# Performance work log

Hardware: AMD Instinct MI355X
Metric: run time of the kernel (lower is better)

The kernel has to match this reference:

```python
import jax, jax.numpy as jnp
import numpy as np
import math

IN_C, OUT_C, KH, KW = 128, 128, 3, 3
GROUPS_NUM, NUM_W = 8, 8
STRIDE, PAD, DIL = 1, 1, 1
BETA = 1.0


def setup_inputs() -> dict:
    key = jax.random.key(0)
    ks = jax.random.split(key, 6)
    B, H, W = 8, 56, 56
    n = IN_C * KH * KW
    bound = math.sqrt(6.0 / n)  # reset_parameters bound for weight templates
    inputs = jax.random.normal(ks[0], (B, IN_C, H, W), jnp.float32)
    mask = jax.random.randint(ks[1], (B, H, W), 0, GROUPS_NUM)
    Alpha = jax.random.uniform(ks[2], (B, GROUPS_NUM, H, W), jnp.float32)
    weight_templates = jax.random.uniform(ks[3], (OUT_C * IN_C * KH * KW, NUM_W), jnp.float32, -bound, bound)
    routing_w = jax.random.normal(ks[4], (GROUPS_NUM * NUM_W, IN_C), jnp.float32) * 0.01
    routing_b = jnp.zeros((GROUPS_NUM * NUM_W,), jnp.float32)
    bias = jnp.zeros((OUT_C,), jnp.float32)
    return dict(inputs=inputs, mask=mask, Alpha=Alpha, weight_templates=weight_templates,
                routing_w=routing_w, routing_b=routing_b, bias=bias, use_alpha=1)


def _unfold(x):
    # torch F.unfold-compatible im2col: [B, C*KH*KW, Ho, Wo], channel-major feature order
    return jax.lax.conv_general_dilated_patches(
        x, (KH, KW), (STRIDE, STRIDE), [(PAD, PAD), (PAD, PAD)],
        rhs_dilation=(DIL, DIL), dimension_numbers=('NCHW', 'OIHW', 'NCHW'))


def reference(inputs, mask, Alpha, weight_templates, routing_w, routing_b, bias, use_alpha):
    B, C, H, W = inputs.shape
    K = IN_C * KH * KW
    # SE-style routing: GAP -> fc -> scaled sigmoid (alpha=1.0 in source)
    x_se = inputs.reshape(B, C, -1).mean(-1)                              # [B, C]
    x_se = 2.0 * jax.nn.sigmoid(x_se @ routing_w.T + routing_b) / NUM_W   # [B, G*num_W]
    # blend weight templates: F.linear(x_se.reshape(-1,num_W), weight)
    w = x_se.reshape(B * GROUPS_NUM, NUM_W) @ weight_templates.T          # [B*G, O*K]
    w = w.reshape(B, GROUPS_NUM, OUT_C, K).transpose(0, 2, 3, 1)          # [B, O, K, G]
    patches = _unfold(inputs)                                             # [B, K, Ho, Wo]
    # per-group convolution outputs, then per-pixel group routing
    y = jnp.einsum('bokg,bkhw->boghw', w, patches)                        # [B, O, G, Ho, Wo]
    if use_alpha:
        probs = jax.nn.softmax(BETA * Alpha, axis=1)                      # soft routing [B, G, Ho, Wo]
    else:
        probs = jax.nn.one_hot(mask, GROUPS_NUM, axis=1, dtype=y.dtype)   # hard per-pixel group select
    out = jnp.einsum('boghw,bghw->bohw', y, probs)
    return out + bias.reshape(1, -1, 1, 1)
```

## Files before the change

### kernel.cpp

```cpp
#include <hip/hip_runtime.h>
#include <stdint.h>

#define IN_C   128
#define OUT_C  128
#define KTOT   1152
#define NG     8
#define NW     8
#define NB     8
#define HH     56
#define WWID   56
#define NPIX   3136
#define PPAD   3200
#define MTOT   1024
#define HALO   58
#define HPIX   (HALO*HALO)


typedef __attribute__((ext_vector_type(8))) short short8;
typedef __attribute__((ext_vector_type(8))) unsigned short ushort8;
typedef __attribute__((ext_vector_type(4))) float f32x4;

__device__ __forceinline__ unsigned short f2bf(float f) {
    unsigned u = __float_as_uint(f);
    u += 0x7FFF + ((u >> 16) & 1);
    return (unsigned short)(u >> 16);
}

__device__ __forceinline__ void cp16(const unsigned short* g, unsigned short* l) {
    __builtin_amdgcn_global_load_lds(
        (const __attribute__((address_space(1))) unsigned int*)g,
        (__attribute__((address_space(3))) unsigned int*)l,
        16, 0, 0);
}

__global__ __launch_bounds__(256) void prep_kernel(const float* __restrict__ in,
                                                   const float* __restrict__ T,
                                                   float* __restrict__ xse,
                                                   unsigned short* __restrict__ Apack,
                                                   unsigned short* __restrict__ Xt) {
    __shared__ __align__(16) unsigned char smem[32768];
    const int blk = blockIdx.x;
    const int t = threadIdx.x;

    if (blk < 1024) {
        const float* src = in + (size_t)blk * NPIX;
        float s = 0.f;
        for (int i = t; i < NPIX / 4; i += 256) {
            float4 v = ((const float4*)src)[i];
            s += v.x + v.y + v.z + v.w;
        }
        #pragma unroll
        for (int off = 32; off; off >>= 1) s += __shfl_down(s, off);
        float* ws4 = (float*)smem;
        if ((t & 63) == 0) ws4[t >> 6] = s;
        __syncthreads();
        if (t == 0)
            xse[blk] = (ws4[0] + ws4[1] + ws4[2] + ws4[3]) * (1.0f / (float)NPIX);
        return;
    }
    if (blk < 1152) {
        unsigned short* lh = (unsigned short*)smem;
        const int o = blk - 1024;
        const float* To = T + (size_t)o * 9216;
        #pragma unroll
        for (int it = 0; it < 9; it++) {
            const int f = it * 256 + t;
            const float4 v = ((const float4*)To)[f];
            ushort4 h;
            h.x = f2bf(v.x); h.y = f2bf(v.y); h.z = f2bf(v.z); h.w = f2bf(v.w);
            *(ushort4*)&lh[f * 4] = h;
        }
        __syncthreads();
        const int m16b = o >> 1;
        const int lrb = (o & 1) * 8;
        #pragma unroll
        for (int it = 0; it < 5; it++) {
            const int ch = it * 256 + t;
            if (ch < 1152) {
                const int j = ch & 7, kc = ch >> 3;
                const int s = kc >> 4, c0 = (kc & 15) << 3;
                const int kt = kc >> 2, lq = kc & 3;
                ushort8 v;
                #pragma unroll
                for (int i = 0; i < 8; i++)
                    v[i] = lh[((c0 + i) * 9 + s) * 8 + j];
                const size_t off = ((((size_t)m16b * 36 + kt) * 4 + lq) * 16 + lrb + j) * 8;
                *(ushort8*)&Apack[off] = v;
            }
        }
        return;
    }
    unsigned short* tile = (unsigned short*)smem;
    const int idx = blk - 1152;
    const int yt = idx % 28;
    const int b  = idx / 28;
    const int y0 = yt * 2;

    #pragma unroll
    for (int it = 0; it < 14; it++) {
        const int f = it * 256 + t;
        const int c = f / 28;
        const int rem = f - c * 28;
        const int y = rem / 14;
        const int x4 = rem - y * 14;
        const float4 v = *(const float4*)(in + ((size_t)(b * IN_C + c)) * NPIX
                                          + (y0 + y) * WWID + x4 * 4);
        unsigned short bf0 = f2bf(v.x), bf1 = f2bf(v.y), bf2 = f2bf(v.z), bf3 = f2bf(v.w);
        const int ppb = (y * WWID + x4 * 4) ^ (((c >> 3) & 15) << 2);
        uint2 pk;
        pk.x = (unsigned)bf0 | ((unsigned)bf1 << 16);
        pk.y = (unsigned)bf2 | ((unsigned)bf3 << 16);
        *(uint2*)&tile[c * 128 + ppb] = pk;
    }
    __syncthreads();

    #pragma unroll
    for (int it = 0; it < 7; it++) {
        const int ch = it * 256 + t;
        const int oct = ch & 15;
        const int pp = ch >> 4;
        const int sw = oct << 2;
        ushort8 v;
        #pragma unroll
        for (int i = 0; i < 8; i++)
            v[i] = tile[(oct * 8 + i) * 128 + (pp ^ sw)];
        const int y2 = (pp >= WWID) ? 1 : 0;
        const int xg = pp - y2 * WWID;
        const size_t hp = (size_t)b * HPIX + (y0 + y2 + 1) * HALO + (xg + 1);
        *(ushort8*)&Xt[hp * 128 + oct * 8] = v;
    }

    if (t < 64) {
        const int pi = t >> 4, oct = t & 15;
        const int yy = y0 + 1 + (pi >> 1);
        const int xx = (pi & 1) * 57;
        *(ushort8*)&Xt[((size_t)b * HPIX + yy * HALO + xx) * 128 + oct * 8] =
            (ushort8){0, 0, 0, 0, 0, 0, 0, 0};
    }
    if (yt == 0 || yt == 27) {
        const int yy = (yt == 0) ? 0 : 57;
        #pragma unroll
        for (int it = 0; it < 4; it++) {
            const int ch = it * 256 + t;
            if (ch < 928) {
                const int xx = ch >> 4, oct = ch & 15;
                *(ushort8*)&Xt[((size_t)b * HPIX + yy * HALO + xx) * 128 + oct * 8] =
                    (ushort8){0, 0, 0, 0, 0, 0, 0, 0};
            }
        }
    }
}

__global__ __launch_bounds__(256) void s_kernel(const float* __restrict__ Alpha,
                                                const int* __restrict__ mask,
                                                const float* __restrict__ xse,
                                                const float* __restrict__ rw,
                                                const float* __restrict__ rb,
                                                const int* __restrict__ use_alpha,
                                                float* __restrict__ Sws) {
    const int b = blockIdx.y;
    const int t = threadIdx.x;
    const int p = blockIdx.x * 256 + t;
    __shared__ float xs[IN_C];
    __shared__ float rsh[64];
    if (t < IN_C) xs[t] = xse[b * IN_C + t];
    __syncthreads();
    if (t < 64) {
        float acc = rb[t];
        #pragma unroll 8
        for (int c = 0; c < IN_C; c++) acc += xs[c] * rw[t * IN_C + c];
        rsh[t] = 0.25f / (1.0f + expf(-acc));
    }
    __syncthreads();
    if (p >= PPAD) return;
    float sj[8] = {0, 0, 0, 0, 0, 0, 0, 0};
    if (p < NPIX) {
        float pr[8];
        if (use_alpha[0]) {
            float a[8], m = -1e30f;
            #pragma unroll
            for (int g = 0; g < 8; g++) {
                a[g] = Alpha[((size_t)(b * NG + g)) * NPIX + p];
                m = fmaxf(m, a[g]);
            }
            float sum = 0.f;
            #pragma unroll
            for (int g = 0; g < 8; g++) { pr[g] = expf(a[g] - m); sum += pr[g]; }
            float inv = 1.f / sum;
            #pragma unroll
            for (int g = 0; g < 8; g++) pr[g] *= inv;
        } else {
            int mg = mask[(size_t)b * NPIX + p];
            #pragma unroll
            for (int g = 0; g < 8; g++) pr[g] = (g == mg) ? 1.f : 0.f;
        }
        #pragma unroll
        for (int g = 0; g < 8; g++)
            #pragma unroll
            for (int j = 0; j < 8; j++) sj[j] += pr[g] * rsh[g * 8 + j];
    }
    float* dst = Sws + ((size_t)b * PPAD + p) * 8;
    *(f32x4*)dst = (f32x4){sj[0], sj[1], sj[2], sj[3]};
    *(f32x4*)(dst + 4) = (f32x4){sj[4], sj[5], sj[6], sj[7]};
}

__global__ __launch_bounds__(256) void gemm_kernel(const unsigned short* __restrict__ Apack,
                                                   const unsigned short* __restrict__ Xt,
                                                   const float* __restrict__ Sws,
                                                   const float* __restrict__ bias,
                                                   float* __restrict__ out) {
    __shared__ __align__(16) unsigned short Bsh[4][512 * 8];
    const int tid = threadIdx.x;
    const int wv = tid >> 6, ln = tid & 63;
    const int lq = ln >> 4, lr = ln & 15;
    const int wrow = wv >> 1, wcol = wv & 1;

    const int lid = blockIdx.x;
    const int b   = lid & 7;
    const int sl  = lid >> 3;
    const int mt  = sl & 7;
    const int nt  = sl >> 3;

    f32x4 acc[4][4];
    #pragma unroll
    for (int i = 0; i < 4; i++)
        #pragma unroll
        for (int j = 0; j < 4; j++) acc[i][j] = (f32x4){0.f, 0.f, 0.f, 0.f};

    const int js = tid & 3;
    const int r0 = tid >> 2,  q0 = js ^ (r0 & 3) ^ ((r0 >> 2) & 3);
    const int r1 = r0 + 64,   q1 = js ^ (r1 & 3) ^ ((r1 >> 2) & 3);
    const int p0 = min(nt * 128 + r0, NPIX - 1);
    const int p1 = min(nt * 128 + r1, NPIX - 1);
    const int y0p = p0 / WWID, x0p = p0 - y0p * WWID;
    const int y1p = p1 / WWID, x1p = p1 - y1p * WWID;
    const unsigned short* gb0 = Xt + ((size_t)b * HPIX + y0p * HALO + x0p) * 128 + q0 * 8;
    const unsigned short* gb1 = Xt + ((size_t)b * HPIX + y1p * HALO + x1p) * 128 + q1 * 8;
    unsigned short* lbA[4];
    #pragma unroll
    for (int i = 0; i < 4; i++) lbA[i] = &Bsh[i][(wv * 64) * 8];

    const unsigned short* gaw[4];
    #pragma unroll
    for (int tm = 0; tm < 4; tm++) {
        const int m16 = mt * 8 + wrow * 4 + tm;
        gaw[tm] = Apack + ((size_t)m16 * 36 * 64 + ln) * 8;
    }

    const int jj = lq ^ (lr & 3) ^ ((lr >> 2) & 3);

    cp16(gb0, lbA[0]); cp16(gb1, lbA[0] + 256 * 8);
    cp16(gb0 + 32, lbA[1]); cp16(gb1 + 32, lbA[1] + 256 * 8);
    short8 af[2][4];
    #pragma unroll
    for (int tm = 0; tm < 4; tm++) af[0][tm] = *(const short8*)(gaw[tm]);
    #pragma unroll
    for (int tm = 0; tm < 4; tm++) af[1][tm] = *(const short8*)(gaw[tm] + 512);

    #pragma unroll 1
    for (int pr = 0; pr < 18; pr++) {
        __syncthreads();
        const int st2 = pr * 2 + 2, st3 = pr * 2 + 3;
        if (pr < 17) {
            const int nk2 = st2 * 32, s2 = nk2 >> 7;
            const int kh2 = s2 / 3, kw2 = s2 - 3 * kh2;
            const int off2 = (kh2 * HALO + kw2) * 128 + (nk2 & 127);
            const int nk3 = st3 * 32, s3 = nk3 >> 7;
            const int kh3 = s3 / 3, kw3 = s3 - 3 * kh3;
            const int off3 = (kh3 * HALO + kw3) * 128 + (nk3 & 127);
            unsigned short* d2 = lbA[st2 & 3];
            unsigned short* d3 = lbA[st3 & 3];
            cp16(gb0 + off2, d2); cp16(gb1 + off2, d2 + 256 * 8);
            cp16(gb0 + off3, d3); cp16(gb1 + off3, d3 + 256 * 8);
        }
        const int bufa = (pr & 1) * 2;
        {
            short8 bfr[4];
            #pragma unroll
            for (int tn = 0; tn < 4; tn++) {
                const int row = wcol * 64 + tn * 16 + lr;
                bfr[tn] = *(const short8*)&Bsh[bufa][(row * 4 + jj) * 8];
            }
            #pragma unroll
            for (int tm = 0; tm < 4; tm++)
                #pragma unroll
                for (int tn = 0; tn < 4; tn++)
                    acc[tm][tn] = __builtin_amdgcn_mfma_f32_16x16x32_bf16(
                        af[0][tm], bfr[tn], acc[tm][tn], 0, 0, 0);
        }
        if (pr < 17) {
            #pragma unroll
            for (int tm = 0; tm < 4; tm++)
                af[0][tm] = *(const short8*)(gaw[tm] + (size_t)st2 * 512);
        }
        {
            short8 bfr[4];
            #pragma unroll
            for (int tn = 0; tn < 4; tn++) {
                const int row = wcol * 64 + tn * 16 + lr;
                bfr[tn] = *(const short8*)&Bsh[bufa + 1][(row * 4 + jj) * 8];
            }
            #pragma unroll
            for (int tm = 0; tm < 4; tm++)
                #pragma unroll
                for (int tn = 0; tn < 4; tn++)
                    acc[tm][tn] = __builtin_amdgcn_mfma_f32_16x16x32_bf16(
                        af[1][tm], bfr[tn], acc[tm][tn], 0, 0, 0);
        }
        if (pr < 17) {
            #pragma unroll
            for (int tm = 0; tm < 4; tm++)
                af[1][tm] = *(const short8*)(gaw[tm] + (size_t)st3 * 512);
        }
    }

    const int j0 = (lq & 1) * 4;
    const int oo = lq >> 1;
    #pragma unroll
    for (int tm = 0; tm < 4; tm++) {
        const int o = mt * 16 + wrow * 8 + tm * 2 + oo;
        const float bo = bias[o];
        #pragma unroll
        for (int tn = 0; tn < 4; tn++) {
            const int p = nt * 128 + wcol * 64 + tn * 16 + lr;
            const f32x4 sv = *(const f32x4*)&Sws[((size_t)b * PPAD + p) * 8 + j0];
            const f32x4 a = acc[tm][tn];
            float part = a.x * sv.x + a.y * sv.y + a.z * sv.z + a.w * sv.w;
            float tot = part + __shfl_xor(part, 16);
            if ((lq & 1) == 0 && p < NPIX)
                out[((size_t)b * OUT_C + o) * NPIX + p] = tot + bo;
        }
    }
}

extern "C" void kernel_launch(void* const* d_in, const int* in_sizes, int n_in,
                              void* d_out, int out_size, void* d_ws, size_t ws_size,
                              hipStream_t stream) {
    const float* inputs = (const float*)d_in[0];
    const int*   mask   = (const int*)d_in[1];
    const float* Alpha  = (const float*)d_in[2];
    const float* wtmpl  = (const float*)d_in[3];
    const float* rw     = (const float*)d_in[4];
    const float* rb     = (const float*)d_in[5];
    const float* bias   = (const float*)d_in[6];
    const int*   ua     = (const int*)d_in[7];
    float* out = (float*)d_out;

    char* ws = (char*)d_ws;
    unsigned short* Xt  = (unsigned short*)ws;
    unsigned short* Apk = (unsigned short*)(ws + 6889472);
    float*          Sws = (float*)(ws + 9248768);
    float*          xse = (float*)(ws + 10067968);

    prep_kernel<<<1376, 256, 0, stream>>>(inputs, wtmpl, xse, Apk, Xt);
    s_kernel<<<dim3(13, NB), 256, 0, stream>>>(Alpha, mask, xse, rw, rb, ua, Sws);
    gemm_kernel<<<1600, 256, 0, stream>>>(Apk, Xt, Sws, bias, out);
}
```

Baseline: 165.6 us.

## Fuse GAP into transpose tiles and routing weights into GEMM prologue

Computes the per-channel global average pool from the bf16 tiles already loaded in the transpose blocks, using atomicAdd into a zeroed buffer, instead of rereading the input in separate blocks. Removes the separate routing/softmax kernel: each GEMM block recomputes the SE routing FC and per-pixel softmax mixing into shared memory. This saves an input pass, a launch and the Sws workspace round-trip. In exchange it adds redundant per-block FC work, a memset, atomics, and a GAP computed on bf16-rounded values.

```diff
diff --git a/kernel.cpp b/kernel.cpp
--- a/kernel.cpp
+++ b/kernel.cpp
@@ -10,7 +10,6 @@
 #define HH     56
 #define WWID   56
 #define NPIX   3136
-#define PPAD   3200
 #define MTOT   1024
 #define HALO   58
 #define HPIX   (HALO*HALO)
@@ -24,6 +23,11 @@
     unsigned u = __float_as_uint(f);
     u += 0x7FFF + ((u >> 16) & 1);
     return (unsigned short)(u >> 16);
+}
+
+__device__ __forceinline__ float bf2f(unsigned short h) {
+    unsigned u = ((unsigned)h) << 16;
+    return __uint_as_float(u);
 }
 
 __device__ __forceinline__ void cp16(const unsigned short* g, unsigned short* l) {
@@ -42,25 +46,9 @@
     const int blk = blockIdx.x;
     const int t = threadIdx.x;
 
-    if (blk < 1024) {
-        const float* src = in + (size_t)blk * NPIX;
-        float s = 0.f;
-        for (int i = t; i < NPIX / 4; i += 256) {
-            float4 v = ((const float4*)src)[i];
-            s += v.x + v.y + v.z + v.w;
-        }
-        #pragma unroll
-        for (int off = 32; off; off >>= 1) s += __shfl_down(s, off);
-        float* ws4 = (float*)smem;
-        if ((t & 63) == 0) ws4[t >> 6] = s;
-        __syncthreads();
-        if (t == 0)
-            xse[blk] = (ws4[0] + ws4[1] + ws4[2] + ws4[3]) * (1.0f / (float)NPIX);
-        return;
-    }
-    if (blk < 1152) {
+    if (blk < 128) {
         unsigned short* lh = (unsigned short*)smem;
-        const int o = blk - 1024;
+        const int o = blk;
         const float* To = T + (size_t)o * 9216;
         #pragma unroll
         for (int it = 0; it < 9; it++) {
@@ -91,7 +79,7 @@
         return;
     }
     unsigned short* tile = (unsigned short*)smem;
-    const int idx = blk - 1152;
+    const int idx = blk - 128;
     const int yt = idx % 28;
     const int b  = idx / 28;
     const int y0 = yt * 2;
@@ -130,6 +118,19 @@
         *(ushort8*)&Xt[hp * 128 + oct * 8] = v;
     }
 
+    if (t < 128) {
+        const int c = t;
+        const int swc = ((c >> 3) & 15) << 2;
+        float s = 0.f;
+        #pragma unroll 8
+        for (int i = 0; i < 112; i++) {
+            int pp = i + (c & 15);
+            if (pp >= 112) pp -= 112;
+            s += bf2f(tile[c * 128 + (pp ^ swc)]);
+        }
+        atomicAdd(&xse[b * IN_C + c], s);
+    }
+
     if (t < 64) {
         const int pi = t >> 4, oct = t & 15;
         const int yy = y0 + 1 + (pi >> 1);
@@ -151,65 +152,21 @@
     }
 }
 
-__global__ __launch_bounds__(256) void s_kernel(const float* __restrict__ Alpha,
-                                                const int* __restrict__ mask,
-                                                const float* __restrict__ xse,
-                                                const float* __restrict__ rw,
-                                                const float* __restrict__ rb,
-                                                const int* __restrict__ use_alpha,
-                                                float* __restrict__ Sws) {
-    const int b = blockIdx.y;
-    const int t = threadIdx.x;
-    const int p = blockIdx.x * 256 + t;
-    __shared__ float xs[IN_C];
-    __shared__ float rsh[64];
-    if (t < IN_C) xs[t] = xse[b * IN_C + t];
-    __syncthreads();
-    if (t < 64) {
-        float acc = rb[t];
-        #pragma unroll 8
-        for (int c = 0; c < IN_C; c++) acc += xs[c] * rw[t * IN_C + c];
-        rsh[t] = 0.25f / (1.0f + expf(-acc));
-    }
-    __syncthreads();
-    if (p >= PPAD) return;
-    float sj[8] = {0, 0, 0, 0, 0, 0, 0, 0};
-    if (p < NPIX) {
-        float pr[8];
-        if (use_alpha[0]) {
-            float a[8], m = -1e30f;
-            #pragma unroll
-            for (int g = 0; g < 8; g++) {
-                a[g] = Alpha[((size_t)(b * NG + g)) * NPIX + p];
-                m = fmaxf(m, a[g]);
-            }
-            float sum = 0.f;
-            #pragma unroll
-            for (int g = 0; g < 8; g++) { pr[g] = expf(a[g] - m); sum += pr[g]; }
-            float inv = 1.f / sum;
-            #pragma unroll
-            for (int g = 0; g < 8; g++) pr[g] *= inv;
-        } else {
-            int mg = mask[(size_t)b * NPIX + p];
-            #pragma unroll
-            for (int g = 0; g < 8; g++) pr[g] = (g == mg) ? 1.f : 0.f;
-        }
-        #pragma unroll
-        for (int g = 0; g < 8; g++)
-            #pragma unroll
-            for (int j = 0; j < 8; j++) sj[j] += pr[g] * rsh[g * 8 + j];
-    }
-    float* dst = Sws + ((size_t)b * PPAD + p) * 8;
-    *(f32x4*)dst = (f32x4){sj[0], sj[1], sj[2], sj[3]};
-    *(f32x4*)(dst + 4) = (f32x4){sj[4], sj[5], sj[6], sj[7]};
-}
-
 __global__ __launch_bounds__(256) void gemm_kernel(const unsigned short* __restrict__ Apack,
                                                    const unsigned short* __restrict__ Xt,
-                                                   const float* __restrict__ Sws,
+                                                   const float* __restrict__ xse,
+                                                   const float* __restrict__ rw,
+                                                   const float* __restrict__ rb,
+                                                   const float* __restrict__ Alpha,
+                                                   const int* __restrict__ mask,
+                                                   const int* __restrict__ use_alpha,
                                                    const float* __restrict__ bias,
                                                    float* __restrict__ out) {
     __shared__ __align__(16) unsigned short Bsh[4][512 * 8];
+    __shared__ float ssh[128 * 8];
+    __shared__ float xs[IN_C];
+    __shared__ float rsh[64];
+
     const int tid = threadIdx.x;
     const int wv = tid >> 6, ln = tid & 63;
     const int lq = ln >> 4, lr = ln & 15;
@@ -220,12 +177,6 @@
     const int sl  = lid >> 3;
     const int mt  = sl & 7;
     const int nt  = sl >> 3;
-
-    f32x4 acc[4][4];
-    #pragma unroll
-    for (int i = 0; i < 4; i++)
-        #pragma unroll
-        for (int j = 0; j < 4; j++) acc[i][j] = (f32x4){0.f, 0.f, 0.f, 0.f};
 
     const int js = tid & 3;
     const int r0 = tid >> 2,  q0 = js ^ (r0 & 3) ^ ((r0 >> 2) & 3);
@@ -249,6 +200,16 @@
 
     const int jj = lq ^ (lr & 3) ^ ((lr >> 2) & 3);
 
+    if (tid < IN_C) xs[tid] = xse[b * IN_C + tid] * (1.0f / (float)NPIX);
+    __syncthreads();
+    if (tid < 64) {
+        float acc = rb[tid];
+        #pragma unroll 8
+        for (int c = 0; c < IN_C; c++) acc += xs[c] * rw[tid * IN_C + c];
+        rsh[tid] = 0.25f / (1.0f + expf(-acc));
+    }
+    __syncthreads();
+
     cp16(gb0, lbA[0]); cp16(gb1, lbA[0] + 256 * 8);
     cp16(gb0 + 32, lbA[1]); cp16(gb1 + 32, lbA[1] + 256 * 8);
     short8 af[2][4];
@@ -256,6 +217,43 @@
     for (int tm = 0; tm < 4; tm++) af[0][tm] = *(const short8*)(gaw[tm]);
     #pragma unroll
     for (int tm = 0; tm < 4; tm++) af[1][tm] = *(const short8*)(gaw[tm] + 512);
+
+    if (tid < 128) {
+        const int p = nt * 128 + tid;
+        float sj[8] = {0, 0, 0, 0, 0, 0, 0, 0};
+        if (p < NPIX) {
+            if (use_alpha[0]) {
+                float a[8], m = -1e30f;
+                #pragma unroll
+                for (int g = 0; g < 8; g++) {
+                    a[g] = Alpha[((size_t)(b * NG + g)) * NPIX + p];
+                    m = fmaxf(m, a[g]);
+                }
+                float pr[8], sum = 0.f;
+                #pragma unroll
+                for (int g = 0; g < 8; g++) { pr[g] = expf(a[g] - m); sum += pr[g]; }
+                const float inv = 1.f / sum;
+                #pragma unroll
+                for (int g = 0; g < 8; g++) {
+                    const float w = pr[g] * inv;
+                    #pragma unroll
+                    for (int j = 0; j < 8; j++) sj[j] += w * rsh[g * 8 + j];
+                }
+            } else {
+                const int mg = mask[(size_t)b * NPIX + p];
+                #pragma unroll
+                for (int j = 0; j < 8; j++) sj[j] = rsh[mg * 8 + j];
+            }
+        }
+        #pragma unroll
+        for (int j = 0; j < 8; j++) ssh[tid * 8 + j] = sj[j];
+    }
+
+    f32x4 acc[4][4];
+    #pragma unroll
+    for (int i = 0; i < 4; i++)
+        #pragma unroll
+        for (int j = 0; j < 4; j++) acc[i][j] = (f32x4){0.f, 0.f, 0.f, 0.f};
 
     #pragma unroll 1
     for (int pr = 0; pr < 18; pr++) {
@@ -322,8 +320,9 @@
         const float bo = bias[o];
         #pragma unroll
         for (int tn = 0; tn < 4; tn++) {
-            const int p = nt * 128 + wcol * 64 + tn * 16 + lr;
-            const f32x4 sv = *(const f32x4*)&Sws[((size_t)b * PPAD + p) * 8 + j0];
+            const int pp = wcol * 64 + tn * 16 + lr;
+            const int p = nt * 128 + pp;
+            const f32x4 sv = *(const f32x4*)&ssh[pp * 8 + j0];
             const f32x4 a = acc[tm][tn];
             float part = a.x * sv.x + a.y * sv.y + a.z * sv.z + a.w * sv.w;
             float tot = part + __shfl_xor(part, 16);
@@ -349,10 +348,9 @@
     char* ws = (char*)d_ws;
     unsigned short* Xt  = (unsigned short*)ws;
     unsigned short* Apk = (unsigned short*)(ws + 6889472);
-    float*          Sws = (float*)(ws + 9248768);
-    float*          xse = (float*)(ws + 10067968);
-
-    prep_kernel<<<1376, 256, 0, stream>>>(inputs, wtmpl, xse, Apk, Xt);
-    s_kernel<<<dim3(13, NB), 256, 0, stream>>>(Alpha, mask, xse, rw, rb, ua, Sws);
-    gemm_kernel<<<1600, 256, 0, stream>>>(Apk, Xt, Sws, bias, out);
-}
+    float*          xse = (float*)(ws + 9248768);
+
+    hipMemsetAsync(xse, 0, IN_C * NB * sizeof(float), stream);
+    prep_kernel<<<352, 256, 0, stream>>>(inputs, wtmpl, xse, Apk, Xt);
+    gemm_kernel<<<1600, 256, 0, stream>>>(Apk, Xt, xse, rw, rb, Alpha, mask, ua, bias, out);
+}
```

After: 174.3 us. 5.2% more time.
